# Kernel optimization log

Measured on AMD Instinct MI355X. Metric: run time of the kernel, lower is better.

## Reference

```python
import jax, jax.numpy as jnp
import numpy as np

DIM_M = 4
DIM_C = 4   # context dim
DIM_F = 4   # feature dim
DIM_Q = DIM_F + 1  # [scale | features]
B = 2_000_000


def setup_inputs() -> dict:
    key = jax.random.key(0)
    k1, k2, k3, k4 = jax.random.split(key, 4)
    xss = jax.random.normal(k1, (B, DIM_M, DIM_Q), dtype=jnp.float32)
    # ragged lengths in [1, DIM_M]
    seq_lengths = jax.random.randint(k2, (B,), 1, DIM_M + 1, dtype=jnp.int64)
    # torch.nn.Linear default init ~ U(-1/sqrt(fan_in), 1/sqrt(fan_in)); any small init is fine for a reference
    W_cob = jax.random.normal(k3, (DIM_C, DIM_F), dtype=jnp.float32) / np.sqrt(DIM_F).astype(np.float32)
    W_reg = jax.random.normal(k4, (DIM_M, DIM_C), dtype=jnp.float32) / np.sqrt(DIM_C).astype(np.float32)
    return {"xss": xss, "seq_lengths": seq_lengths, "W_cob": W_cob, "W_reg": W_reg}


def reference(xss, seq_lengths, W_cob, W_reg):
    # xss: [B, S, Q] with S = DIM_M, Q = DIM_F + 1
    scales = xss[..., 0:1]            # [B, S, 1]
    fs = xss[..., 1:]                 # [B, S, F]
    bs = jnp.einsum('bsf,cf->bsc', fs, W_cob)          # change_of_basis (no bias)
    valid = jnp.arange(DIM_M)[None, :] < seq_lengths[:, None]   # [B, S] ragged mask
    cs = bs * scales * valid[..., None].astype(bs.dtype)        # base_coordinates, masked
    context = cs.sum(axis=1)                                    # pool over valid prefix -> [B, C]
    ys = jnp.einsum('bc,mc->bm', context, W_reg)
    projs = jnp.einsum('bsm,bm->bs', bs, ys)                    # per-position dot with broadcast ys
    # ragged concat: only valid positions, in batch-major order (matches torch.cat of per-batch slices)
    return projs[valid][:, None]                                # [sum(seq_lengths), 1]
```

## Files before the change

kernel.cpp:

```cpp
#include <hip/hip_runtime.h>

#define NT 256

__global__ __launch_bounds__(NT) void sum_kernel(const int* __restrict__ seq,
                                                 unsigned* __restrict__ blockSums,
                                                 int n) {
    __shared__ unsigned wsum[4];
    int tid = threadIdx.x;
    int gid = blockIdx.x * NT + tid;
    int lane = tid & 63, wave = tid >> 6;
    unsigned v = (gid < n) ? (unsigned)seq[gid] : 0u;
    #pragma unroll
    for (int off = 32; off > 0; off >>= 1) v += __shfl_down(v, off);
    if (lane == 0) wsum[wave] = v;
    __syncthreads();
    if (tid == 0) blockSums[blockIdx.x] = wsum[0] + wsum[1] + wsum[2] + wsum[3];
}

__device__ __forceinline__ unsigned block_excl_scan(unsigned v_in, int tid,
                                                    unsigned* wtot ,
                                                    unsigned* block_total) {
    int lane = tid & 63, wave = tid >> 6;
    unsigned v = v_in;
    #pragma unroll
    for (int off = 1; off < 64; off <<= 1) {
        unsigned t = __shfl_up(v, off);
        if (lane >= off) v += t;
    }
    if (lane == 63) wtot[wave] = v;
    __syncthreads();
    unsigned woff = 0;
    #pragma unroll
    for (int w = 0; w < 4; w++) woff += (w < wave) ? wtot[w] : 0u;
    if (block_total) *block_total = wtot[0] + wtot[1] + wtot[2] + wtot[3];
    return woff + v - v_in;
}

__global__ __launch_bounds__(NT) void group_scan_kernel(const unsigned* __restrict__ blockSums,
                                                        unsigned* __restrict__ blockOffsets,
                                                        unsigned* __restrict__ groupSums,
                                                        int nb) {
    __shared__ unsigned wtot[4];
    int tid = threadIdx.x;
    int i = blockIdx.x * NT + tid;
    unsigned v = (i < nb) ? blockSums[i] : 0u;
    unsigned total;
    unsigned excl = block_excl_scan(v, tid, wtot, &total);
    if (i < nb) blockOffsets[i] = excl;
    if (tid == 0) groupSums[blockIdx.x] = total;
}

__global__ __launch_bounds__(64) void top_scan_kernel(const unsigned* __restrict__ groupSums,
                                                      unsigned* __restrict__ groupOffsets,
                                                      int ng) {
    int tid = threadIdx.x;
    unsigned v = (tid < ng) ? groupSums[tid] : 0u;
    unsigned incl = v;
    #pragma unroll
    for (int off = 1; off < 64; off <<= 1) {
        unsigned t = __shfl_up(incl, off);
        if (tid >= off) incl += t;
    }
    if (tid < ng) groupOffsets[tid] = incl - v;
}

__global__ __launch_bounds__(NT) void main_kernel(const float* __restrict__ xss,
                                                  const int* __restrict__ seq,
                                                  const float* __restrict__ Wcob,
                                                  const float* __restrict__ Wreg,
                                                  const unsigned* __restrict__ blockOffsets,
                                                  const unsigned* __restrict__ groupOffsets,
                                                  float* __restrict__ out,
                                                  int n) {
    __shared__ unsigned wtot[4];
    int tid = threadIdx.x;
    int gid = blockIdx.x * NT + tid;
    unsigned L = (gid < n) ? (unsigned)seq[gid] : 0u;

    unsigned excl = block_excl_scan(L, tid, wtot, nullptr);
    unsigned offset = groupOffsets[blockIdx.x >> 8] + blockOffsets[blockIdx.x] + excl;

    if (gid >= n) return;

    const float* p = xss + (size_t)gid * 20;
    float4 v0 = *(const float4*)(p + 0);
    float4 v1 = *(const float4*)(p + 4);
    float4 v2 = *(const float4*)(p + 8);
    float4 v3 = *(const float4*)(p + 12);
    float4 v4 = *(const float4*)(p + 16);
    float x[20];
    x[0]=v0.x;  x[1]=v0.y;  x[2]=v0.z;  x[3]=v0.w;
    x[4]=v1.x;  x[5]=v1.y;  x[6]=v1.z;  x[7]=v1.w;
    x[8]=v2.x;  x[9]=v2.y;  x[10]=v2.z; x[11]=v2.w;
    x[12]=v3.x; x[13]=v3.y; x[14]=v3.z; x[15]=v3.w;
    x[16]=v4.x; x[17]=v4.y; x[18]=v4.z; x[19]=v4.w;

    float wc[16], wr[16];
    #pragma unroll
    for (int i = 0; i < 16; i++) { wc[i] = Wcob[i]; wr[i] = Wreg[i]; }

    float bs[4][4];
    #pragma unroll
    for (int s = 0; s < 4; s++) {
        #pragma unroll
        for (int c = 0; c < 4; c++) {
            float acc = 0.f;
            #pragma unroll
            for (int f = 0; f < 4; f++) acc += x[s * 5 + 1 + f] * wc[c * 4 + f];
            bs[s][c] = acc;
        }
    }

    float ctx[4] = {0.f, 0.f, 0.f, 0.f};
    #pragma unroll
    for (int s = 0; s < 4; s++) {
        float m = (s < (int)L) ? x[s * 5] : 0.f;
        #pragma unroll
        for (int c = 0; c < 4; c++) ctx[c] += bs[s][c] * m;
    }

    float ys[4];
    #pragma unroll
    for (int m = 0; m < 4; m++) {
        float acc = 0.f;
        #pragma unroll
        for (int c = 0; c < 4; c++) acc += ctx[c] * wr[m * 4 + c];
        ys[m] = acc;
    }

    #pragma unroll
    for (int s = 0; s < 4; s++) {
        if (s < (int)L) {
            float acc = 0.f;
            #pragma unroll
            for (int m = 0; m < 4; m++) acc += bs[s][m] * ys[m];
            out[offset + s] = acc;
        }
    }
}

extern "C" void kernel_launch(void* const* d_in, const int* in_sizes, int n_in,
                              void* d_out, int out_size, void* d_ws, size_t ws_size,
                              hipStream_t stream) {
    const float* xss  = (const float*)d_in[0];
    const int*   seq  = (const int*)d_in[1];
    const float* Wcob = (const float*)d_in[2];
    const float* Wreg = (const float*)d_in[3];
    float* out = (float*)d_out;

    int n  = in_sizes[1];
    int nb = (n + NT - 1) / NT;
    int ng = (nb + NT - 1) / NT;

    unsigned* blockSums    = (unsigned*)d_ws;
    unsigned* blockOffsets = blockSums + nb;
    unsigned* groupSums    = blockOffsets + nb;
    unsigned* groupOffsets = groupSums + ng;

    sum_kernel<<<nb, NT, 0, stream>>>(seq, blockSums, n);
    group_scan_kernel<<<ng, NT, 0, stream>>>(blockSums, blockOffsets, groupSums, nb);
    top_scan_kernel<<<1, 64, 0, stream>>>(groupSums, groupOffsets, ng);
    main_kernel<<<nb, NT, 0, stream>>>(xss, seq, Wcob, Wreg, blockOffsets, groupOffsets, out, n);
}
```

Before: 247.7 us.

## Fuse ragged scan and compute into single-pass decoupled look-back kernel

Replaces the three-kernel hierarchical prefix sum plus main kernel with one kernel that uses a dynamic block counter and decoupled look-back, where one wave scans 64 predecessors' status flags at a time. Outputs are staged in shared memory and written as a contiguous coalesced block. This removes a separate pass over seq_lengths and several kernel launches, and improves the store pattern. The cost is serialized inter-block dependency chains and spin-waiting, plus a small init kernel. Status words pack the flag into 2 bits and the sum into 30 bits.

New measurement: 295.8 us. +19.4%, slower.

```diff
diff --git a/kernel.cpp b/kernel.cpp
--- a/kernel.cpp
+++ b/kernel.cpp
@@ -2,26 +2,50 @@
 
 #define NT 256
 
-__global__ __launch_bounds__(NT) void sum_kernel(const int* __restrict__ seq,
-                                                 unsigned* __restrict__ blockSums,
-                                                 int n) {
-    __shared__ unsigned wsum[4];
-    int tid = threadIdx.x;
-    int gid = blockIdx.x * NT + tid;
-    int lane = tid & 63, wave = tid >> 6;
-    unsigned v = (gid < n) ? (unsigned)seq[gid] : 0u;
-    #pragma unroll
-    for (int off = 32; off > 0; off >>= 1) v += __shfl_down(v, off);
-    if (lane == 0) wsum[wave] = v;
-    __syncthreads();
-    if (tid == 0) blockSums[blockIdx.x] = wsum[0] + wsum[1] + wsum[2] + wsum[3];
+#define FLAG_INV 0u
+#define FLAG_AGG 1u
+#define FLAG_PRE 2u
+
+__global__ __launch_bounds__(NT) void init_status(unsigned* __restrict__ status, int nb) {
+    int i = blockIdx.x * NT + threadIdx.x;
+    if (i < nb + 1) status[i] = 0u;
 }
 
-__device__ __forceinline__ unsigned block_excl_scan(unsigned v_in, int tid,
-                                                    unsigned* wtot ,
-                                                    unsigned* block_total) {
-    int lane = tid & 63, wave = tid >> 6;
-    unsigned v = v_in;
+__global__ __launch_bounds__(NT) void fused_kernel(const float* __restrict__ xss,
+                                                   const int* __restrict__ seq,
+                                                   const float* __restrict__ Wcob,
+                                                   const float* __restrict__ Wreg,
+                                                   unsigned* __restrict__ ws,
+                                                   float* __restrict__ out,
+                                                   int n) {
+    unsigned* counter = ws;
+    unsigned* status  = ws + 1;
+
+    __shared__ unsigned wtot[4];
+    __shared__ unsigned s_bid;
+    __shared__ unsigned s_excl;
+    __shared__ float outbuf[NT * 4];
+
+    const int tid  = threadIdx.x;
+    const int lane = tid & 63;
+    const int wave = tid >> 6;
+
+    if (tid == 0) s_bid = atomicAdd(counter, 1u);
+    __syncthreads();
+    const int bid = (int)s_bid;
+    const int gid = bid * NT + tid;
+
+    unsigned L = (gid < n) ? (unsigned)seq[gid] : 0u;
+
+    const int cgid = (gid < n) ? gid : (n - 1);
+    const float* p = xss + (size_t)cgid * 20;
+    float4 v0 = *(const float4*)(p + 0);
+    float4 v1 = *(const float4*)(p + 4);
+    float4 v2 = *(const float4*)(p + 8);
+    float4 v3 = *(const float4*)(p + 12);
+    float4 v4 = *(const float4*)(p + 16);
+
+    unsigned v = L;
     #pragma unroll
     for (int off = 1; off < 64; off <<= 1) {
         unsigned t = __shfl_up(v, off);
@@ -32,72 +56,62 @@
     unsigned woff = 0;
     #pragma unroll
     for (int w = 0; w < 4; w++) woff += (w < wave) ? wtot[w] : 0u;
-    if (block_total) *block_total = wtot[0] + wtot[1] + wtot[2] + wtot[3];
-    return woff + v - v_in;
-}
+    const unsigned total      = wtot[0] + wtot[1] + wtot[2] + wtot[3];
+    const unsigned excl_local = woff + v - L;
 
-__global__ __launch_bounds__(NT) void group_scan_kernel(const unsigned* __restrict__ blockSums,
-                                                        unsigned* __restrict__ blockOffsets,
-                                                        unsigned* __restrict__ groupSums,
-                                                        int nb) {
-    __shared__ unsigned wtot[4];
-    int tid = threadIdx.x;
-    int i = blockIdx.x * NT + tid;
-    unsigned v = (i < nb) ? blockSums[i] : 0u;
-    unsigned total;
-    unsigned excl = block_excl_scan(v, tid, wtot, &total);
-    if (i < nb) blockOffsets[i] = excl;
-    if (tid == 0) groupSums[blockIdx.x] = total;
-}
+    if (tid == 0) {
+        unsigned word = ((bid == 0) ? (FLAG_PRE << 30) : (FLAG_AGG << 30)) | total;
+        __hip_atomic_store(&status[bid], word, __ATOMIC_RELAXED, __HIP_MEMORY_SCOPE_AGENT);
+        if (bid == 0) s_excl = 0u;
+    }
 
-__global__ __launch_bounds__(64) void top_scan_kernel(const unsigned* __restrict__ groupSums,
-                                                      unsigned* __restrict__ groupOffsets,
-                                                      int ng) {
-    int tid = threadIdx.x;
-    unsigned v = (tid < ng) ? groupSums[tid] : 0u;
-    unsigned incl = v;
+    if (bid > 0 && tid < 64) {
+        unsigned run = 0;
+        int j = bid;
+        for (;;) {
+            int idx = j - 64 + tid;
+            unsigned s = (idx >= 0)
+                ? __hip_atomic_load(&status[idx], __ATOMIC_RELAXED, __HIP_MEMORY_SCOPE_AGENT)
+                : (FLAG_PRE << 30);
+            unsigned flag = s >> 30;
+            unsigned long long bal_inv = __ballot(flag == FLAG_INV);
+            unsigned long long bal_pre = __ballot(flag == FLAG_PRE);
+            int hi = (bal_inv == 0ull) ? -1 : (63 - __clzll(bal_inv));
+            int hp = (bal_pre == 0ull) ? -1 : (63 - __clzll(bal_pre));
+            if (hp > hi) {
+                unsigned c = (tid >= hp) ? (s & 0x3FFFFFFFu) : 0u;
+                #pragma unroll
+                for (int off = 32; off > 0; off >>= 1) c += __shfl_down(c, off);
+                run += __shfl(c, 0);
+                break;
+            } else if (hi < 0) {
+                unsigned c = s & 0x3FFFFFFFu;
+                #pragma unroll
+                for (int off = 32; off > 0; off >>= 1) c += __shfl_down(c, off);
+                run += __shfl(c, 0);
+                j -= 64;
+            } else {
+                __builtin_amdgcn_s_sleep(1);
+            }
+        }
+        if (tid == 0) {
+            __hip_atomic_store(&status[bid],
+                               (FLAG_PRE << 30) | ((run + total) & 0x3FFFFFFFu),
+                               __ATOMIC_RELAXED, __HIP_MEMORY_SCOPE_AGENT);
+            s_excl = run;
+        }
+    }
+
+    float wc[16], wr[16];
     #pragma unroll
-    for (int off = 1; off < 64; off <<= 1) {
-        unsigned t = __shfl_up(incl, off);
-        if (tid >= off) incl += t;
-    }
-    if (tid < ng) groupOffsets[tid] = incl - v;
-}
+    for (int i = 0; i < 16; i++) { wc[i] = Wcob[i]; wr[i] = Wreg[i]; }
 
-__global__ __launch_bounds__(NT) void main_kernel(const float* __restrict__ xss,
-                                                  const int* __restrict__ seq,
-                                                  const float* __restrict__ Wcob,
-                                                  const float* __restrict__ Wreg,
-                                                  const unsigned* __restrict__ blockOffsets,
-                                                  const unsigned* __restrict__ groupOffsets,
-                                                  float* __restrict__ out,
-                                                  int n) {
-    __shared__ unsigned wtot[4];
-    int tid = threadIdx.x;
-    int gid = blockIdx.x * NT + tid;
-    unsigned L = (gid < n) ? (unsigned)seq[gid] : 0u;
-
-    unsigned excl = block_excl_scan(L, tid, wtot, nullptr);
-    unsigned offset = groupOffsets[blockIdx.x >> 8] + blockOffsets[blockIdx.x] + excl;
-
-    if (gid >= n) return;
-
-    const float* p = xss + (size_t)gid * 20;
-    float4 v0 = *(const float4*)(p + 0);
-    float4 v1 = *(const float4*)(p + 4);
-    float4 v2 = *(const float4*)(p + 8);
-    float4 v3 = *(const float4*)(p + 12);
-    float4 v4 = *(const float4*)(p + 16);
     float x[20];
     x[0]=v0.x;  x[1]=v0.y;  x[2]=v0.z;  x[3]=v0.w;
     x[4]=v1.x;  x[5]=v1.y;  x[6]=v1.z;  x[7]=v1.w;
     x[8]=v2.x;  x[9]=v2.y;  x[10]=v2.z; x[11]=v2.w;
     x[12]=v3.x; x[13]=v3.y; x[14]=v3.z; x[15]=v3.w;
     x[16]=v4.x; x[17]=v4.y; x[18]=v4.z; x[19]=v4.w;
-
-    float wc[16], wr[16];
-    #pragma unroll
-    for (int i = 0; i < 16; i++) { wc[i] = Wcob[i]; wr[i] = Wreg[i]; }
 
     float bs[4][4];
     #pragma unroll
@@ -134,9 +148,14 @@
             float acc = 0.f;
             #pragma unroll
             for (int m = 0; m < 4; m++) acc += bs[s][m] * ys[m];
-            out[offset + s] = acc;
+            outbuf[excl_local + s] = acc;
         }
     }
+
+    __syncthreads();
+    const unsigned base = s_excl;
+    for (unsigned i = tid; i < total; i += NT)
+        out[base + i] = outbuf[i];
 }
 
 extern "C" void kernel_launch(void* const* d_in, const int* in_sizes, int n_in,
@@ -150,15 +169,10 @@
 
     int n  = in_sizes[1];
     int nb = (n + NT - 1) / NT;
-    int ng = (nb + NT - 1) / NT;
 
-    unsigned* blockSums    = (unsigned*)d_ws;
-    unsigned* blockOffsets = blockSums + nb;
-    unsigned* groupSums    = blockOffsets + nb;
-    unsigned* groupOffsets = groupSums + ng;
+    unsigned* ws = (unsigned*)d_ws;
 
-    sum_kernel<<<nb, NT, 0, stream>>>(seq, blockSums, n);
-    group_scan_kernel<<<ng, NT, 0, stream>>>(blockSums, blockOffsets, groupSums, nb);
-    top_scan_kernel<<<1, 64, 0, stream>>>(groupSums, groupOffsets, ng);
-    main_kernel<<<nb, NT, 0, stream>>>(xss, seq, Wcob, Wreg, blockOffsets, groupOffsets, out, n);
+    int ib = (nb + 1 + NT - 1) / NT;
+    init_status<<<ib, NT, 0, stream>>>(ws, nb);
+    fused_kernel<<<nb, NT, 0, stream>>>(xss, seq, Wcob, Wreg, ws, out, n);
 }
```

## Collapse three-level scan into tile sums plus in-kernel prefix reduction

Applied to the files above, without the earlier changes.

Replaces the three-kernel hierarchical prefix scan with one tile-sum kernel. The main kernel then computes its block prefix by reducing all earlier block totals itself. Each thread now handles four consecutive batch elements, loaded with a vectorised int4 read of the lengths, which cuts the number of blocks and so the redundant prefix reduction. This removes two kernel launches and their serial dependencies. In exchange, xss loads and output stores are less coalesced across threads, and later blocks do extra prefix reads.

After: 271.4 us. 1.1x slower.

```diff
diff --git a/kernel.cpp b/kernel.cpp
--- a/kernel.cpp
+++ b/kernel.cpp
@@ -1,27 +1,61 @@
 #include <hip/hip_runtime.h>
 
 #define NT 256
+#define EPT 4
+#define BLK_ELEMS (NT * EPT)
 
-__global__ __launch_bounds__(NT) void sum_kernel(const int* __restrict__ seq,
-                                                 unsigned* __restrict__ blockSums,
-                                                 int n) {
+__global__ __launch_bounds__(NT) void tile_sum_kernel(const int* __restrict__ seq,
+                                                      unsigned* __restrict__ blockTotal,
+                                                      int n) {
     __shared__ unsigned wsum[4];
-    int tid = threadIdx.x;
-    int gid = blockIdx.x * NT + tid;
-    int lane = tid & 63, wave = tid >> 6;
-    unsigned v = (gid < n) ? (unsigned)seq[gid] : 0u;
+    const int tid = threadIdx.x, lane = tid & 63, wave = tid >> 6;
+    const int base = blockIdx.x * BLK_ELEMS + tid * EPT;
+    unsigned v = 0;
+    if (base + EPT <= n) {
+        int4 q = *(const int4*)(seq + base);
+        v = (unsigned)(q.x + q.y + q.z + q.w);
+    } else {
+        for (int e = 0; e < EPT; e++)
+            if (base + e < n) v += (unsigned)seq[base + e];
+    }
     #pragma unroll
     for (int off = 32; off > 0; off >>= 1) v += __shfl_down(v, off);
     if (lane == 0) wsum[wave] = v;
     __syncthreads();
-    if (tid == 0) blockSums[blockIdx.x] = wsum[0] + wsum[1] + wsum[2] + wsum[3];
+    if (tid == 0) blockTotal[blockIdx.x] = wsum[0] + wsum[1] + wsum[2] + wsum[3];
 }
 
-__device__ __forceinline__ unsigned block_excl_scan(unsigned v_in, int tid,
-                                                    unsigned* wtot ,
-                                                    unsigned* block_total) {
-    int lane = tid & 63, wave = tid >> 6;
-    unsigned v = v_in;
+__global__ __launch_bounds__(NT) void main_kernel(const float* __restrict__ xss,
+                                                  const int* __restrict__ seq,
+                                                  const float* __restrict__ Wcob,
+                                                  const float* __restrict__ Wreg,
+                                                  const unsigned* __restrict__ blockTotal,
+                                                  float* __restrict__ out,
+                                                  int n) {
+    __shared__ unsigned wred[4];
+    __shared__ unsigned wtot[4];
+    const int tid = threadIdx.x, lane = tid & 63, wave = tid >> 6;
+    const int bid = blockIdx.x;
+    const int base = bid * BLK_ELEMS + tid * EPT;
+
+    int l[EPT];
+    if (base + EPT <= n) {
+        int4 q = *(const int4*)(seq + base);
+        l[0] = q.x; l[1] = q.y; l[2] = q.z; l[3] = q.w;
+    } else {
+        #pragma unroll
+        for (int e = 0; e < EPT; e++) l[e] = (base + e < n) ? seq[base + e] : 0;
+    }
+    const unsigned tsum = (unsigned)(l[0] + l[1] + l[2] + l[3]);
+
+    unsigned acc = 0;
+    for (int i = tid; i < bid; i += NT) acc += blockTotal[i];
+    unsigned r = acc;
+    #pragma unroll
+    for (int off = 32; off > 0; off >>= 1) r += __shfl_down(r, off);
+    if (lane == 0) wred[wave] = r;
+
+    unsigned v = tsum;
     #pragma unroll
     for (int off = 1; off < 64; off <<= 1) {
         unsigned t = __shfl_up(v, off);
@@ -29,112 +63,70 @@
     }
     if (lane == 63) wtot[wave] = v;
     __syncthreads();
+    const unsigned prefix = wred[0] + wred[1] + wred[2] + wred[3];
     unsigned woff = 0;
     #pragma unroll
     for (int w = 0; w < 4; w++) woff += (w < wave) ? wtot[w] : 0u;
-    if (block_total) *block_total = wtot[0] + wtot[1] + wtot[2] + wtot[3];
-    return woff + v - v_in;
-}
-
-__global__ __launch_bounds__(NT) void group_scan_kernel(const unsigned* __restrict__ blockSums,
-                                                        unsigned* __restrict__ blockOffsets,
-                                                        unsigned* __restrict__ groupSums,
-                                                        int nb) {
-    __shared__ unsigned wtot[4];
-    int tid = threadIdx.x;
-    int i = blockIdx.x * NT + tid;
-    unsigned v = (i < nb) ? blockSums[i] : 0u;
-    unsigned total;
-    unsigned excl = block_excl_scan(v, tid, wtot, &total);
-    if (i < nb) blockOffsets[i] = excl;
-    if (tid == 0) groupSums[blockIdx.x] = total;
-}
-
-__global__ __launch_bounds__(64) void top_scan_kernel(const unsigned* __restrict__ groupSums,
-                                                      unsigned* __restrict__ groupOffsets,
-                                                      int ng) {
-    int tid = threadIdx.x;
-    unsigned v = (tid < ng) ? groupSums[tid] : 0u;
-    unsigned incl = v;
-    #pragma unroll
-    for (int off = 1; off < 64; off <<= 1) {
-        unsigned t = __shfl_up(incl, off);
-        if (tid >= off) incl += t;
-    }
-    if (tid < ng) groupOffsets[tid] = incl - v;
-}
-
-__global__ __launch_bounds__(NT) void main_kernel(const float* __restrict__ xss,
-                                                  const int* __restrict__ seq,
-                                                  const float* __restrict__ Wcob,
-                                                  const float* __restrict__ Wreg,
-                                                  const unsigned* __restrict__ blockOffsets,
-                                                  const unsigned* __restrict__ groupOffsets,
-                                                  float* __restrict__ out,
-                                                  int n) {
-    __shared__ unsigned wtot[4];
-    int tid = threadIdx.x;
-    int gid = blockIdx.x * NT + tid;
-    unsigned L = (gid < n) ? (unsigned)seq[gid] : 0u;
-
-    unsigned excl = block_excl_scan(L, tid, wtot, nullptr);
-    unsigned offset = groupOffsets[blockIdx.x >> 8] + blockOffsets[blockIdx.x] + excl;
-
-    if (gid >= n) return;
-
-    const float* p = xss + (size_t)gid * 20;
-    float4 v0 = *(const float4*)(p + 0);
-    float4 v1 = *(const float4*)(p + 4);
-    float4 v2 = *(const float4*)(p + 8);
-    float4 v3 = *(const float4*)(p + 12);
-    float4 v4 = *(const float4*)(p + 16);
-    float x[20];
-    x[0]=v0.x;  x[1]=v0.y;  x[2]=v0.z;  x[3]=v0.w;
-    x[4]=v1.x;  x[5]=v1.y;  x[6]=v1.z;  x[7]=v1.w;
-    x[8]=v2.x;  x[9]=v2.y;  x[10]=v2.z; x[11]=v2.w;
-    x[12]=v3.x; x[13]=v3.y; x[14]=v3.z; x[15]=v3.w;
-    x[16]=v4.x; x[17]=v4.y; x[18]=v4.z; x[19]=v4.w;
+    unsigned o = prefix + woff + (v - tsum);
 
     float wc[16], wr[16];
     #pragma unroll
     for (int i = 0; i < 16; i++) { wc[i] = Wcob[i]; wr[i] = Wreg[i]; }
 
-    float bs[4][4];
     #pragma unroll
-    for (int s = 0; s < 4; s++) {
-        #pragma unroll
-        for (int c = 0; c < 4; c++) {
-            float acc = 0.f;
+    for (int e = 0; e < EPT; e++) {
+        const int gid = base + e;
+        const int L = l[e];
+        if (gid < n && L > 0) {
+            const float* p = xss + (size_t)gid * 20;
+            float4 v0 = *(const float4*)(p + 0);
+            float4 v1 = *(const float4*)(p + 4);
+            float4 v2 = *(const float4*)(p + 8);
+            float4 v3 = *(const float4*)(p + 12);
+            float4 v4 = *(const float4*)(p + 16);
+            float x[20];
+            x[0]=v0.x;  x[1]=v0.y;  x[2]=v0.z;  x[3]=v0.w;
+            x[4]=v1.x;  x[5]=v1.y;  x[6]=v1.z;  x[7]=v1.w;
+            x[8]=v2.x;  x[9]=v2.y;  x[10]=v2.z; x[11]=v2.w;
+            x[12]=v3.x; x[13]=v3.y; x[14]=v3.z; x[15]=v3.w;
+            x[16]=v4.x; x[17]=v4.y; x[18]=v4.z; x[19]=v4.w;
+
+            float bs[4][4];
             #pragma unroll
-            for (int f = 0; f < 4; f++) acc += x[s * 5 + 1 + f] * wc[c * 4 + f];
-            bs[s][c] = acc;
-        }
-    }
-
-    float ctx[4] = {0.f, 0.f, 0.f, 0.f};
-    #pragma unroll
-    for (int s = 0; s < 4; s++) {
-        float m = (s < (int)L) ? x[s * 5] : 0.f;
-        #pragma unroll
-        for (int c = 0; c < 4; c++) ctx[c] += bs[s][c] * m;
-    }
-
-    float ys[4];
-    #pragma unroll
-    for (int m = 0; m < 4; m++) {
-        float acc = 0.f;
-        #pragma unroll
-        for (int c = 0; c < 4; c++) acc += ctx[c] * wr[m * 4 + c];
-        ys[m] = acc;
-    }
-
-    #pragma unroll
-    for (int s = 0; s < 4; s++) {
-        if (s < (int)L) {
-            float acc = 0.f;
+            for (int s = 0; s < 4; s++) {
+                #pragma unroll
+                for (int c = 0; c < 4; c++) {
+                    float a = 0.f;
+                    #pragma unroll
+                    for (int f = 0; f < 4; f++) a += x[s * 5 + 1 + f] * wc[c * 4 + f];
+                    bs[s][c] = a;
+                }
+            }
+            float ctx[4] = {0.f, 0.f, 0.f, 0.f};
             #pragma unroll
-            for (int m = 0; m < 4; m++) acc += bs[s][m] * ys[m];
-            out[offset + s] = acc;
+            for (int s = 0; s < 4; s++) {
+                float m = (s < L) ? x[s * 5] : 0.f;
+                #pragma unroll
+                for (int c = 0; c < 4; c++) ctx[c] += bs[s][c] * m;
+            }
+            float ys[4];
+            #pragma unroll
+            for (int m = 0; m < 4; m++) {
+                float a = 0.f;
+                #pragma unroll
+                for (int c = 0; c < 4; c++) a += ctx[c] * wr[m * 4 + c];
+                ys[m] = a;
+            }
+            #pragma unroll
+            for (int s = 0; s < 4; s++) {
+                if (s < L) {
+                    float a = 0.f;
+                    #pragma unroll
+                    for (int m = 0; m < 4; m++) a += bs[s][m] * ys[m];
+                    out[o + s] = a;
+                }
+            }
+            o += (unsigned)L;
         }
     }
 }
@@ -149,16 +141,10 @@
     float* out = (float*)d_out;
 
     int n  = in_sizes[1];
-    int nb = (n + NT - 1) / NT;
-    int ng = (nb + NT - 1) / NT;
+    int nb = (n + BLK_ELEMS - 1) / BLK_ELEMS;
 
-    unsigned* blockSums    = (unsigned*)d_ws;
-    unsigned* blockOffsets = blockSums + nb;
-    unsigned* groupSums    = blockOffsets + nb;
-    unsigned* groupOffsets = groupSums + ng;
+    unsigned* blockTotal = (unsigned*)d_ws;
 
-    sum_kernel<<<nb, NT, 0, stream>>>(seq, blockSums, n);
-    group_scan_kernel<<<ng, NT, 0, stream>>>(blockSums, blockOffsets, groupSums, nb);
-    top_scan_kernel<<<1, 64, 0, stream>>>(groupSums, groupOffsets, ng);
-    main_kernel<<<nb, NT, 0, stream>>>(xss, seq, Wcob, Wreg, blockOffsets, groupOffsets, out, n);
+    tile_sum_kernel<<<nb, NT, 0, stream>>>(seq, blockTotal, n);
+    main_kernel<<<nb, NT, 0, stream>>>(xss, seq, Wcob, Wreg, blockTotal, out, n);
 }
```
